# Optimization experiments

Hardware: AMD Instinct MI355X
Metric: run time of the kernel (lower is better)

## Reference

```python
import jax, jax.numpy as jnp
import numpy as np
from jax import lax
from jax.scipy.special import gammaln

B, S, I, H, T, C, LOC, K, P = 64, 256, 512, 80, 600, 512, 8, 21, 11
A_PRIOR, B_PRIOR = 0.1, 0.9
DN = ('NCH', 'OIH', 'NCH')  # 1D conv dimension numbers


def _beta_binom_prior():
    # beta-binomial pmf over P points (n = P-1), flipped to match the torch buffer
    n = float(P - 1)
    k = jnp.arange(P, dtype=jnp.float32)
    lpmf = (gammaln(n + 1.0) - gammaln(k + 1.0) - gammaln(n - k + 1.0)
            + gammaln(k + A_PRIOR) + gammaln(n - k + B_PRIOR) - gammaln(n + A_PRIOR + B_PRIOR)
            - (gammaln(A_PRIOR) + gammaln(B_PRIOR) - gammaln(A_PRIOR + B_PRIOR)))
    return jnp.exp(lpmf)[::-1]


def setup_inputs() -> dict:
    key = jax.random.key(0)
    ks = jax.random.split(key, 10)
    sc = jnp.float32(0.05)
    return {
        'encodings': jax.random.normal(ks[0], (B, S, I), jnp.float32),
        'mask': jnp.ones((B, S), jnp.float32),
        'gt': jax.random.normal(ks[1], (B, T, H), jnp.float32),
        'gru_wi': jax.random.normal(ks[2], (3 * C, I + H), jnp.float32) * sc,
        'gru_wh': jax.random.normal(ks[3], (3 * C, C), jnp.float32) * sc,
        'gru_bi': jnp.zeros((3 * C,), jnp.float32),
        'gru_bh': jnp.zeros((3 * C,), jnp.float32),
        'loc_conv_w': jax.random.normal(ks[4], (LOC, 1, K), jnp.float32) * sc,
        'loc_proj_w': jax.random.normal(ks[5], (C // 2, LOC), jnp.float32) * sc,
        'kernel_w1': jax.random.normal(ks[6], (C, C), jnp.float32) * sc,
        'kernel_b1': jnp.zeros((C,), jnp.float32),
        'kernel_w2': jax.random.normal(ks[7], (LOC * K, C), jnp.float32) * sc,
        'dyn_w': jax.random.normal(ks[8], (C // 2, LOC), jnp.float32) * sc,
        'dyn_b': jnp.zeros((C // 2,), jnp.float32),
        'agg_w': jax.random.normal(ks[9], (C // 2,), jnp.float32) * sc,
        'prior': _beta_binom_prior(),
    }


def reference(encodings, mask, gt, gru_wi, gru_wh, gru_bi, gru_bh,
              loc_conv_w, loc_proj_w, kernel_w1, kernel_b1, kernel_w2,
              dyn_w, dyn_b, agg_w, prior):
    b, s, _ = encodings.shape
    loc, _, k = loc_conv_w.shape
    p = prior.shape[0]
    h0 = jnp.zeros((b, gru_wh.shape[1]), encodings.dtype)
    a0 = jnp.zeros((b, s), encodings.dtype).at[:, 0].set(1.0)

    def step(carry, frame):
        state, alpha = carry
        # attention context from previous alignment
        prev = jnp.einsum('bsi,bs->bi', encodings, alpha)
        x = jnp.concatenate([frame, prev], axis=-1)
        # torch GRUCell gate math
        gx = x @ gru_wi.T + gru_bi
        gh = state @ gru_wh.T + gru_bh
        xr, xz, xn = jnp.split(gx, 3, axis=-1)
        hr, hz, hn = jnp.split(gh, 3, axis=-1)
        r = jax.nn.sigmoid(xr + hr)
        z = jax.nn.sigmoid(xz + hz)
        n = jnp.tanh(xn + r * hn)
        query = (1.0 - z) * n + z * state
        # dynamic kernels predicted from query: [B*loc, 1, K]
        dkern = (jnp.tanh(query @ kernel_w1.T + kernel_b1) @ kernel_w2.T).reshape(b * loc, 1, k)
        pa = alpha[:, None, :]  # [B,1,S]
        # static location conv: [B,loc,S]
        loc_feat = lax.conv_general_dilated(pa, loc_conv_w, (1,), [(k // 2, k // 2)], dimension_numbers=DN)
        # dynamic conv: grouped conv, one filter set per batch element
        dyn_feat = lax.conv_general_dilated(alpha[None], dkern, (1,), [(k // 2, k // 2)],
                                            dimension_numbers=DN, feature_group_count=b).reshape(b, loc, s)
        score = (jnp.einsum('cl,bls->bcs', loc_proj_w, loc_feat)
                 + jnp.einsum('cl,bls->bcs', dyn_w, dyn_feat)
                 + dyn_b[None, :, None])
        # causal prior conv (kernel is pre-flipped beta-binomial pmf)
        pri = lax.conv_general_dilated(pa, prior[None, None, :], (1,), [(p - 1, 0)], dimension_numbers=DN)[:, 0]
        energy = jnp.einsum('c,bcs->bs', agg_w, jnp.tanh(score)) + jnp.log(pri + 1e-5)
        energy = jnp.where(mask > 0, energy, -jnp.inf)
        new_alpha = jax.nn.softmax(energy, axis=-1)
        return (query, new_alpha), new_alpha

    _, alphas = lax.scan(step, (h0, a0), jnp.swapaxes(gt, 0, 1))  # [T,B,S]
    return jnp.swapaxes(alphas, 0, 1)  # [B,T,S]
```

## Files before the change

### kernel.cpp

```cpp
#include <hip/hip_runtime.h>
#include <hip/hip_bf16.h>

#define Bn 64
#define Sn 256
#define In 512
#define Hn 80
#define Tn 600
#define Cn 512
#define LOCn 8
#define Kn 21
#define Pn 11
#define G3 1536

typedef _Float16 h2 __attribute__((ext_vector_type(2)));

enum : unsigned {
  OFF_WHPK     = 0u,
  OFF_W1PK     = OFF_WHPK + 256u * 1536u,
  OFF_W2PK     = OFF_W1PK + 256u * 512u,
  OFF_WIFPK    = OFF_W2PK + 256u * 168u,
  OFF_WIPREVPK = OFF_WIFPK + 40u * 1536u,
  OFF_BI       = OFF_WIPREVPK + 256u * 1536u,
  OFF_BH       = OFF_BI + 1536u,
  OFF_B1       = OFF_BH + 1536u,
  OFF_LW       = OFF_B1 + 512u,
  OFF_PW       = OFF_LW + 176u,
  OFF_DW       = OFF_PW + 2048u,
  OFF_DB       = OFF_DW + 2048u,
  OFF_AGG      = OFF_DB + 256u,
  OFF_PRI      = OFF_AGG + 256u,
  OFF_FLAG     = OFF_PRI + 16u,
  OFF_WIPT     = 1030400u,
  OFF_ENCW     = OFF_WIPT + 512u * 1536u,
  WS_END_ENCW  = OFF_ENCW + 64u * 128u * 1536u,
  OFF_XH       = WS_END_ENCW,
  OFF_TP       = OFF_XH + 64u * 256u,
  OFF_XE       = OFF_TP + 64u * 4096u,
  OFF_FLG      = OFF_XE + 64u * 256u,
  WS_END_ALL   = OFF_FLG + 64u * 32u
};

__device__ __forceinline__ float ld_any(const void* p, long long i, int bf) {
  if (bf) {
    unsigned v = ((const unsigned short*)p)[i];
    return __uint_as_float(v << 16);
  }
  return ((const float*)p)[i];
}
__device__ __forceinline__ unsigned pack_h2(float a, float b) {
  union { h2 h; unsigned u; } x;
  x.h.x = (_Float16)a; x.h.y = (_Float16)b;
  return x.u;
}
__device__ __forceinline__ h2 u_to_h2(unsigned u) {
  union { h2 h; unsigned u; } x; x.u = u; return x.h;
}
__device__ __forceinline__ float dot2f(unsigned w, unsigned a, float acc) {
#if __has_builtin(__builtin_amdgcn_fdot2)
  return __builtin_amdgcn_fdot2(u_to_h2(w), u_to_h2(a), acc, false);
#else
  h2 wv = u_to_h2(w), av = u_to_h2(a);
  return fmaf((float)wv.x, (float)av.x, fmaf((float)wv.y, (float)av.y, acc));
#endif
}

__device__ __forceinline__ void st_dev(unsigned* p, unsigned v) {
  __hip_atomic_store(p, v, __ATOMIC_RELAXED, __HIP_MEMORY_SCOPE_AGENT);
}
__device__ __forceinline__ unsigned ld_dev(const unsigned* p) {
  return __hip_atomic_load(p, __ATOMIC_RELAXED, __HIP_MEMORY_SCOPE_AGENT);
}

__device__ __forceinline__ float fast_exp(float x) {
  return __builtin_amdgcn_exp2f(x * 1.4426950408889634f);
}
__device__ __forceinline__ float fast_sigmoid(float x) {
  return __builtin_amdgcn_rcpf(1.f + fast_exp(-x));
}
__device__ __forceinline__ float fast_tanh(float x) {
  float u = __builtin_amdgcn_exp2f(x * 2.8853900817779268f);
  return 1.f - 2.f * __builtin_amdgcn_rcpf(u + 1.f);
}
__device__ __forceinline__ float fast_log(float x) {
  return __builtin_amdgcn_logf(x) * 0.6931471805599453f;
}

__global__ void k_flag(const void* mask, float* ws) {
  if (threadIdx.x == 0 && blockIdx.x == 0) {
    unsigned w = *(const unsigned*)mask;
    ((int*)(ws + OFF_FLAG))[0] = (w == 0x3F803F80u) ? 1 : 0;
  }
}

__global__ void k_zero(unsigned* U) {
  int x = blockIdx.x * blockDim.x + threadIdx.x;
  if (x < 64 * 32) U[OFF_FLG + x] = 0u;
}

__global__ void k_prep(const void* wi, const void* wh, const void* gbi, const void* gbh,
                       const void* lcw, const void* lpw, const void* w1, const void* kb1,
                       const void* w2, const void* dw, const void* ddb, const void* aggw,
                       const void* pri, float* wsf, unsigned* U) {
  const int bf = ((const int*)(wsf + OFF_FLAG))[0];
  const int tid = blockIdx.x * blockDim.x + threadIdx.x;
  const int nT = gridDim.x * blockDim.x;
  for (int x = tid; x < 256 * 1536; x += nT) {
    int g = x % 3, y = x / 3, c = y % 512, kp = y / 512;
    long long r = (long long)(g * 512 + c) * Cn + 2 * kp;
    U[OFF_WHPK + x] = pack_h2(ld_any(wh, r, bf), ld_any(wh, r + 1, bf));
  }
  for (int x = tid; x < 256 * 512; x += nT) {
    int c = x % 512, kp = x / 512;
    long long r = (long long)c * Cn + 2 * kp;
    U[OFF_W1PK + x] = pack_h2(ld_any(w1, r, bf), ld_any(w1, r + 1, bf));
  }
  for (int x = tid; x < 256 * 168; x += nT) {
    int j = x % 168, kp = x / 168;
    long long r = (long long)j * Cn + 2 * kp;
    U[OFF_W2PK + x] = pack_h2(ld_any(w2, r, bf), ld_any(w2, r + 1, bf));
  }
  for (int x = tid; x < 40 * 1536; x += nT) {
    int g = x % 3, y = x / 3, c = y % 512, jp = y / 512;
    long long r = (long long)(g * 512 + c) * (In + Hn) + 2 * jp;
    U[OFF_WIFPK + x] = pack_h2(ld_any(wi, r, bf), ld_any(wi, r + 1, bf));
  }
  for (int x = tid; x < 256 * 1536; x += nT) {
    int g = x % 3, y = x / 3, c = y % 512, kp = y / 512;
    long long r = (long long)(g * 512 + c) * (In + Hn) + Hn + 2 * kp;
    U[OFF_WIPREVPK + x] = pack_h2(ld_any(wi, r, bf), ld_any(wi, r + 1, bf));
  }
  for (int x = tid; x < 512 * 1536; x += nT) {
    int i = x / 1536, m = x % 1536;
    wsf[OFF_WIPT + x] = ld_any(wi, (long long)m * (In + Hn) + Hn + i, bf);
  }
  for (int x = tid; x < G3; x += nT) wsf[OFF_BI + x] = ld_any(gbi, x, bf);
  for (int x = tid; x < G3; x += nT) wsf[OFF_BH + x] = ld_any(gbh, x, bf);
  for (int x = tid; x < Cn; x += nT) wsf[OFF_B1 + x] = ld_any(kb1, x, bf);
  for (int x = tid; x < LOCn * Kn; x += nT) wsf[OFF_LW + x] = ld_any(lcw, x, bf);
  for (int x = tid; x < 256 * LOCn; x += nT) wsf[OFF_PW + x] = ld_any(lpw, x, bf);
  for (int x = tid; x < 256 * LOCn; x += nT) wsf[OFF_DW + x] = ld_any(dw, x, bf);
  for (int x = tid; x < 256; x += nT) wsf[OFF_DB + x] = ld_any(ddb, x, bf);
  for (int x = tid; x < 256; x += nT) wsf[OFF_AGG + x] = ld_any(aggw, x, bf);
  for (int x = tid; x < Pn; x += nT) wsf[OFF_PRI + x] = ld_any(pri, x, bf);
}

__global__ __launch_bounds__(1024) void k_encw(const void* __restrict__ enc_,
                                               const float* __restrict__ wsf,
                                               unsigned* __restrict__ U) {
  const int b = blockIdx.x >> 2, chunk = blockIdx.x & 3;
  const int bf = ((const int*)(wsf + OFF_FLAG))[0];
  const int tid = threadIdx.x;
  const int r = tid >> 8, m0 = tid & 255;
  const int s0 = chunk * 64 + r * 16;
  const float* WiPT = wsf + OFF_WIPT;
  for (int g6 = 0; g6 < 6; ++g6) {
    int m = m0 + (g6 << 8);
    float acc[16];
    #pragma unroll
    for (int j = 0; j < 16; ++j) acc[j] = 0.f;
    #pragma unroll 4
    for (int i = 0; i < In; ++i) {
      float w = WiPT[(size_t)i * G3 + m];
      #pragma unroll
      for (int j = 0; j < 16; ++j)
        acc[j] = fmaf(w, ld_any(enc_, ((long long)b * Sn + (s0 + j)) * In + i, bf), acc[j]);
    }
    int cc = m & 511, gg = m >> 9;
    unsigned* dst = U + OFF_ENCW + (size_t)b * 128 * G3;
    #pragma unroll
    for (int jj = 0; jj < 8; ++jj)
      dst[(size_t)(((s0 >> 1) + jj) * 512 + cc) * 3 + gg] = pack_h2(acc[2 * jj], acc[2 * jj + 1]);
  }
}

__global__ __launch_bounds__(1024, 4) void k_split(
    const void* __restrict__ mask_, const void* __restrict__ gt_,
    const float* __restrict__ wsf, unsigned* __restrict__ UW,
    void* __restrict__ out_) {
  const int b = blockIdx.x >> 2;
  const int j = blockIdx.x & 3;
  const int tid = threadIdx.x;
  const int bf = ((const int*)(wsf + OFF_FLAG))[0];

  const float* BI = wsf + OFF_BI;
  const float* BH = wsf + OFF_BH;
  const float* B1 = wsf + OFF_B1;
  const float* lw = wsf + OFF_LW;
  const float* Pw = wsf + OFF_PW;
  const float* Dw = wsf + OFF_DW;
  const float* dbv = wsf + OFF_DB;
  const float* agg = wsf + OFF_AGG;
  const float* prw = wsf + OFF_PRI;
  const unsigned* U = UW;
  const unsigned* encwB = U + OFF_ENCW + (size_t)b * 128 * G3;
  unsigned* XH = UW + OFF_XH + b * 256;
  unsigned* TP = UW + OFF_TP + b * 4096;
  unsigned* XE = UW + OFF_XE + b * 256;
  unsigned* FLG = UW + OFF_FLG + b * 32;

  __shared__ __align__(16) float sA[280];
  __shared__ __align__(16) unsigned sAH[128];
  __shared__ __align__(16) unsigned sXfH[40];
  __shared__ __align__(16) unsigned sHH[256];
  __shared__ __align__(16) unsigned sHsl[64];
  __shared__ __align__(16) unsigned sT1H[256];
  __shared__ __align__(16) float sHfC[128];
  __shared__ __align__(16) float sP[6 * 8 * 128];
  __shared__ __align__(16) float sG6[768];
  __shared__ __align__(16) float sFLo[512];
  __shared__ __align__(16) float sFDo[512];
  __shared__ __align__(16) float sPriL[64];
  __shared__ __align__(16) float sDk[176];
  __shared__ __align__(16) float sMask[256];
  __shared__ float sRed2[8];

  for (int x = tid; x < 280; x += 1024) sA[x] = 0.f;
  for (int x = tid; x < 128; x += 1024) { sAH[x] = 0u; sHfC[x & 127] = 0.f; }
  for (int x = tid; x < 256; x += 1024) { sHH[x] = 0u;
    sMask[x] = ld_any(mask_, (long long)b * Sn + x, bf); }
  if (tid == 0) { sA[10] = 1.f; sAH[0] = pack_h2(1.f, 0.f); }
  if (tid < 40) sXfH[tid] = pack_h2(ld_any(gt_, (long long)b * Tn * Hn + 2 * tid, bf),
                                    ld_any(gt_, (long long)b * Tn * Hn + 2 * tid + 1, bf));
  __syncthreads();

  for (int t = 0; t < Tn; ++t) {
    const unsigned ep = (unsigned)(t + 1);
    {
      const int ks = tid >> 7, cl = tid & 127;
      const int c = (j << 7) + cl;
      float xr = 0.f, xz = 0.f, xn = 0.f, hr = 0.f, hz = 0.f, hn = 0.f;
      const unsigned* pf = U + OFF_WIFPK + 3 * c;
      #pragma unroll
      for (int jp = ks * 5; jp < ks * 5 + 5; ++jp) {
        unsigned a = sXfH[jp];
        xr = dot2f(pf[jp * G3], a, xr);
        xz = dot2f(pf[jp * G3 + 1], a, xz);
        xn = dot2f(pf[jp * G3 + 2], a, xn);
      }
      const unsigned* pe = encwB + 3 * c;
      #pragma unroll 4
      for (int kp = ks * 16; kp < ks * 16 + 16; ++kp) {
        unsigned a = sAH[kp];
        if (a) {
          xr = dot2f(pe[kp * G3], a, xr);
          xz = dot2f(pe[kp * G3 + 1], a, xz);
          xn = dot2f(pe[kp * G3 + 2], a, xn);
        }
      }
      const unsigned* ph = U + OFF_WHPK + 3 * c;
      #pragma unroll 4
      for (int kp = ks * 32; kp < ks * 32 + 32; ++kp) {
        unsigned a = sHH[kp];
        hr = dot2f(ph[kp * G3], a, hr);
        hz = dot2f(ph[kp * G3 + 1], a, hz);
        hn = dot2f(ph[kp * G3 + 2], a, hn);
      }
      sP[(0 * 8 + ks) * 128 + cl] = xr;
      sP[(1 * 8 + ks) * 128 + cl] = xz;
      sP[(2 * 8 + ks) * 128 + cl] = xn;
      sP[(3 * 8 + ks) * 128 + cl] = hr;
      sP[(4 * 8 + ks) * 128 + cl] = hz;
      sP[(5 * 8 + ks) * 128 + cl] = hn;
    }
    __syncthreads();
    if (tid < 768) {
      int g = tid >> 7, cl = tid & 127;
      float s = 0.f;
      #pragma unroll
      for (int ks = 0; ks < 8; ++ks) s += sP[(g * 8 + ks) * 128 + cl];
      sG6[tid] = s;
    }
    __syncthreads();
    if (tid < 128) {
      int cl = tid, c = (j << 7) + cl;
      float xr = sG6[cl] + BI[c];
      float xz = sG6[128 + cl] + BI[512 + c];
      float xn = sG6[256 + cl] + BI[1024 + c];
      float hr = sG6[384 + cl] + BH[c];
      float hz = sG6[512 + cl] + BH[512 + c];
      float hn = sG6[640 + cl] + BH[1024 + c];
      float r = fast_sigmoid(xr + hr);
      float z = fast_sigmoid(xz + hz);
      float n = fast_tanh(xn + r * hn);
      float hN = (1.f - z) * n + z * sHfC[cl];
      sHfC[cl] = hN;
      float nb = __shfl_xor(hN, 1, 64);
      if (!(tid & 1)) sHsl[tid >> 1] = pack_h2(hN, nb);
    } else if (tid >= 192 && tid < 256) {
      int sl = tid - 192;
      float acc = 0.f;
      #pragma unroll
      for (int k = 0; k < Pn; ++k) acc = fmaf(prw[k], sA[(j << 6) + sl + k], acc);
      sPriL[sl] = acc;
    } else if (tid >= 512) {
      int idx = tid - 512;
      int l = __builtin_amdgcn_readfirstlane(idx >> 6), sl = idx & 63;
      float acc = 0.f;
      #pragma unroll
      for (int k = 0; k < Kn; ++k) acc = fmaf(lw[l * Kn + k], sA[(j << 6) + sl + k], acc);
      sFLo[l * 64 + sl] = acc;
    }
    __syncthreads();
    {
      const int c = tid & 511, kh = tid >> 9;
      const unsigned* m1 = U + OFF_W1PK + (unsigned)(j * 64 + kh * 32) * 512 + c;
      float acc = 0.f;
      #pragma unroll 4
      for (int kp = 0; kp < 32; ++kp)
        acc = dot2f(m1[kp * 512], sHsl[kh * 32 + kp], acc);
      st_dev(&TP[(j * 2 + kh) * 512 + c], __float_as_uint(acc));
    }
    if (tid < 64) st_dev(&XH[(j << 6) + tid], sHsl[tid]);
    __syncthreads();
    if (tid == 0) st_dev(&FLG[j], ep);
    if (tid < 4) {
      while (ld_dev(&FLG[tid]) < ep) __builtin_amdgcn_s_sleep(1);
    }
    __syncthreads();
    if (tid < 256) sHH[tid] = ld_dev(&XH[tid]);
    if (tid < 512) {
      float a = B1[tid];
      #pragma unroll
      for (int p = 0; p < 8; ++p) a += __uint_as_float(ld_dev(&TP[p * 512 + tid]));
      float tv = fast_tanh(a);
      float nb = __shfl_xor(tv, 1, 64);
      if (!(tid & 1)) sT1H[tid >> 1] = pack_h2(tv, nb);
    }
    __syncthreads();
    if (tid < 672) {
      int kq = tid / 168, j2 = tid - kq * 168;
      const unsigned* m2 = U + OFF_W2PK + kq * 64 * 168 + j2;
      float acc = 0.f;
      #pragma unroll 4
      for (int kp = 0; kp < 64; ++kp)
        acc = dot2f(m2[kp * 168], sT1H[kq * 64 + kp], acc);
      sP[tid] = acc;
    }
    __syncthreads();
    if (tid < 168) sDk[tid] = sP[tid] + sP[tid + 168] + sP[tid + 336] + sP[tid + 504];
    __syncthreads();
    if (tid < 512) {
      int l = __builtin_amdgcn_readfirstlane(tid >> 6), sl = tid & 63;
      float acc = 0.f;
      #pragma unroll
      for (int k = 0; k < Kn; ++k) acc = fmaf(sDk[l * Kn + k], sA[(j << 6) + sl + k], acc);
      sFDo[l * 64 + sl] = acc;
    }
    __syncthreads();
    {
      const int sl = tid & 63;
      const int slice = __builtin_amdgcn_readfirstlane(tid >> 6);
      float fl[LOCn], fd[LOCn];
      #pragma unroll
      for (int l = 0; l < LOCn; ++l) { fl[l] = sFLo[l * 64 + sl]; fd[l] = sFDo[l * 64 + sl]; }
      float e = 0.f;
      const int c0 = slice << 4;
      for (int c = c0; c < c0 + 16; ++c) {
        float sc = dbv[c];
        #pragma unroll
        for (int l = 0; l < LOCn; ++l) {
          sc = fmaf(Pw[c * LOCn + l], fl[l], sc);
          sc = fmaf(Dw[c * LOCn + l], fd[l], sc);
        }
        e = fmaf(agg[c], fast_tanh(sc), e);
      }
      sP[slice * 64 + sl] = e;
    }
    __syncthreads();
    if (tid < 64) {
      float E = 0.f;
      #pragma unroll
      for (int q = 0; q < 16; ++q) E += sP[q * 64 + tid];
      E += fast_log(sPriL[tid] + 1e-5f);
      if (!(sMask[(j << 6) + tid] > 0.f)) E = -__builtin_inff();
      st_dev(&XE[(j << 6) + tid], __float_as_uint(E));
    }
    __builtin_amdgcn_s_waitcnt(0);
    if (tid == 0) st_dev(&FLG[16 + j], ep);
    if (tid < 4) {
      while (ld_dev(&FLG[16 + tid]) < ep) __builtin_amdgcn_s_sleep(1);
    }
    __syncthreads();
    float eV = -__builtin_inff(), exv = 0.f;
    if (tid < 256) {
      eV = __uint_as_float(ld_dev(&XE[tid]));
      float m = eV;
      #pragma unroll
      for (int off = 32; off > 0; off >>= 1) m = fmaxf(m, __shfl_xor(m, off, 64));
      if ((tid & 63) == 0) sRed2[tid >> 6] = m;
    }
    __syncthreads();
    if (tid < 256) {
      float M = fmaxf(fmaxf(sRed2[0], sRed2[1]), fmaxf(sRed2[2], sRed2[3]));
      exv = fast_exp(eV - M);
      float ssum = exv;
      #pragma unroll
      for (int off = 32; off > 0; off >>= 1) ssum += __shfl_xor(ssum, off, 64);
      if ((tid & 63) == 0) sRed2[4 + (tid >> 6)] = ssum;
    } else if (tid >= 512 && tid < 552 && t + 1 < Tn) {
      int i = tid - 512;
      sXfH[i] = pack_h2(ld_any(gt_, ((long long)b * Tn + t + 1) * Hn + 2 * i, bf),
                        ld_any(gt_, ((long long)b * Tn + t + 1) * Hn + 2 * i + 1, bf));
    }
    __syncthreads();
    if (tid < 256) {
      float Z = sRed2[4] + sRed2[5] + sRed2[6] + sRed2[7];
      float a = exv * __builtin_amdgcn_rcpf(Z);
      sA[10 + tid] = a;
      float nb = __shfl_xor(a, 1, 64);
      if (!(tid & 1)) sAH[tid >> 1] = pack_h2(a, nb);
    }
    __syncthreads();
    if (tid >= 256 && tid < 320) {
      int s = (j << 6) + (tid - 256);
      float a = sA[10 + s];
      size_t oi = ((size_t)b * Tn + t) * Sn + s;
      if (bf) ((__hip_bfloat16*)out_)[oi] = __float2bfloat16(a);
      else ((float*)out_)[oi] = a;
    }
    __syncthreads();
  }
}

__global__ __launch_bounds__(1024) void k_single(
    const void* __restrict__ enc_, const void* __restrict__ mask_,
    const void* __restrict__ gt_, const float* __restrict__ wsf,
    const unsigned* __restrict__ U, void* __restrict__ out_, int use_encw) {
  const int b = blockIdx.x;
  const int tid = threadIdx.x;
  const int bf = ((const int*)(wsf + OFF_FLAG))[0];
  const float* BI = wsf + OFF_BI;
  const float* BH = wsf + OFF_BH;
  const float* B1 = wsf + OFF_B1;
  const float* lw = wsf + OFF_LW;
  const float* Pw = wsf + OFF_PW;
  const float* Dw = wsf + OFF_DW;
  const float* dbv = wsf + OFF_DB;
  const float* agg = wsf + OFF_AGG;
  const float* prw = wsf + OFF_PRI;

  __shared__ __align__(16) float sA[280];
  __shared__ __align__(16) unsigned sAH[128];
  __shared__ __align__(16) unsigned sXfH[40];
  __shared__ __align__(16) unsigned sPrevH[256];
  __shared__ __align__(16) float sHf[512];
  __shared__ __align__(16) unsigned sHH[256];
  __shared__ __align__(16) unsigned sT1H[256];
  __shared__ __align__(16) float sXr[512], sXz[512], sXn[512];
  __shared__ __align__(16) float sHr[512], sHz[512], sHnM[512], sHnP[512];
  __shared__ __align__(16) float sDk[176];
  __shared__ __align__(16) float sFL[LOCn][Sn];
  __shared__ __align__(16) float sFD[LOCn][Sn];
  __shared__ __align__(16) float sPri[Sn];
  __shared__ __align__(16) float sMask[Sn];
  __shared__ __align__(16) float sR[1024];
  __shared__ float sRed2[8];

  for (int x = tid; x < 280; x += 1024) sA[x] = 0.f;
  for (int x = tid; x < 128; x += 1024) sAH[x] = 0u;
  for (int x = tid; x < Cn; x += 1024) sHf[x] = 0.f;
  for (int x = tid; x < 256; x += 1024) sHH[x] = 0u;
  for (int x = tid; x < Sn; x += 1024) sMask[x] = ld_any(mask_, (long long)b * Sn + x, bf);
  if (tid == 0) { sA[Kn / 2] = 1.f; sAH[0] = pack_h2(1.f, 0.f); }
  if (tid < Hn) ((_Float16*)sXfH)[tid] = (_Float16)ld_any(gt_, (long long)b * Tn * Hn + tid, bf);
  __syncthreads();

  const int Pp = use_encw ? 132 : 0;
  const int n3 = 256 - Pp;
  const int n1 = use_encw ? 128 : 256;
  const unsigned* encwB = U + OFF_ENCW + (size_t)b * 128 * G3;

  for (int t = 0; t < Tn; ++t) {
    if (!use_encw) {
      int i = tid & (In - 1);
      int s0 = (tid >> 9) << 7;
      float acc = 0.f;
      if (bf) {
        const unsigned short* enc = (const unsigned short*)enc_ + (size_t)b * Sn * In + i;
        #pragma unroll 4
        for (int s = s0; s < s0 + 128; ++s)
          acc = fmaf(__uint_as_float(((unsigned)enc[(size_t)s * In]) << 16), sA[10 + s], acc);
      } else {
        const float* enc = (const float*)enc_ + (size_t)b * Sn * In + i;
        #pragma unroll 4
        for (int s = s0; s < s0 + 128; ++s)
          acc = fmaf(enc[(size_t)s * In], sA[10 + s], acc);
      }
      sR[tid] = acc;
      __syncthreads();
      if (tid < In) ((_Float16*)sPrevH)[tid] = (_Float16)(sR[tid] + sR[tid + In]);
      __syncthreads();
    }
    if (tid < Cn) {
      const int c = tid;
      float xr = BI[c], xz = BI[c + 512], xn = BI[c + 1024];
      {
        const unsigned* pf = U + OFF_WIFPK + 3 * c;
        #pragma unroll 4
        for (int jp = 0; jp < 40; ++jp) {
          unsigned a = sXfH[jp];
          xr = dot2f(pf[jp * G3], a, xr);
          xz = dot2f(pf[jp * G3 + 1], a, xz);
          xn = dot2f(pf[jp * G3 + 2], a, xn);
        }
      }
      {
        const unsigned* pm = use_encw ? (encwB + 3 * c) : (U + OFF_WIPREVPK + 3 * c);
        const unsigned* aSrc = use_encw ? sAH : sPrevH;
        #pragma unroll 4
        for (int kp = 0; kp < n1; ++kp) {
          unsigned a = aSrc[kp];
          xr = dot2f(pm[kp * G3], a, xr);
          xz = dot2f(pm[kp * G3 + 1], a, xz);
          xn = dot2f(pm[kp * G3 + 2], a, xn);
        }
      }
      {
        float hp = 0.f;
        const unsigned* ph = U + OFF_WHPK + 3 * c + 2;
        #pragma unroll 4
        for (int kp = n3; kp < 256; ++kp)
          hp = dot2f(ph[kp * G3], sHH[kp], hp);
        sHnP[c] = hp;
      }
      sXr[c] = xr; sXz[c] = xz; sXn[c] = xn;
    } else {
      const int c = tid - Cn;
      float hr = BH[c], hz = BH[c + 512], hn = BH[c + 1024];
      const unsigned* ph = U + OFF_WHPK + 3 * c;
      #pragma unroll 4
      for (int kp = 0; kp < n3; ++kp) {
        unsigned a = sHH[kp];
        hr = dot2f(ph[kp * G3], a, hr);
        hz = dot2f(ph[kp * G3 + 1], a, hz);
        hn = dot2f(ph[kp * G3 + 2], a, hn);
      }
      #pragma unroll 4
      for (int kp = n3; kp < 256; ++kp) {
        unsigned a = sHH[kp];
        hr = dot2f(ph[kp * G3], a, hr);
        hz = dot2f(ph[kp * G3 + 1], a, hz);
      }
      sHr[c] = hr; sHz[c] = hz; sHnM[c] = hn;
    }
    __syncthreads();
    if (tid < Cn) {
      int c = tid;
      float r = fast_sigmoid(sXr[c] + sHr[c]);
      float z = fast_sigmoid(sXz[c] + sHz[c]);
      float n = fast_tanh(sXn[c] + r * (sHnM[c] + sHnP[c]));
      float hN = (1.f - z) * n + z * sHf[c];
      sHf[c] = hN;
      ((_Float16*)sHH)[c] = (_Float16)hN;
    } else {
      int j = tid - Cn;
      #pragma unroll
      for (int rr = 0; rr < 4; ++rr) {
        int idx = j + (rr << 9);
        int l = idx >> 8, s = idx & (Sn - 1);
        float acc = 0.f;
        #pragma unroll
        for (int k = 0; k < Kn; ++k) acc = fmaf(lw[l * Kn + k], sA[s + k], acc);
        sFL[l][s] = acc;
      }
      if (j < Sn) {
        float acc = 0.f;
        #pragma unroll
        for (int k = 0; k < Pn; ++k) acc = fmaf(prw[k], sA[j + k], acc);
        sPri[j] = acc;
      }
    }
    __syncthreads();
    {
      int c = tid & (Cn - 1), half = tid >> 9;
      const unsigned* m1 = U + OFF_W1PK + half * 128 * 512 + c;
      float acc = 0.f;
      #pragma unroll 4
      for (int kp = 0; kp < 128; ++kp)
        acc = dot2f(m1[kp * 512], sHH[half * 128 + kp], acc);
      sR[tid] = acc;
    }
    __syncthreads();
    if (tid < Cn) ((_Float16*)sT1H)[tid] = (_Float16)fast_tanh(B1[tid] + sR[tid] + sR[tid + Cn]);
    __syncthreads();
    if (tid < 672) {
      int kq = tid / 168, j = tid - kq * 168;
      const unsigned* m2 = U + OFF_W2PK + kq * 64 * 168 + j;
      float acc = 0.f;
      #pragma unroll 4
      for (int kp = 0; kp < 64; ++kp)
        acc = dot2f(m2[kp * 168], sT1H[kq * 64 + kp], acc);
      sR[tid] = acc;
    }
    __syncthreads();
    if (tid < LOCn * Kn) sDk[tid] = sR[tid] + sR[tid + 168] + sR[tid + 336] + sR[tid + 504];
    __syncthreads();
    #pragma unroll
    for (int rr = 0; rr < 2; ++rr) {
      int idx = tid + (rr << 10);
      int l = idx >> 8, s = idx & (Sn - 1);
      float acc = 0.f;
      #pragma unroll
      for (int k = 0; k < Kn; ++k) acc = fmaf(sDk[l * Kn + k], sA[s + k], acc);
      sFD[l][s] = acc;
    }
    __syncthreads();
    {
      const int q = __builtin_amdgcn_readfirstlane(tid >> 8);
      const int s = tid & (Sn - 1);
      float fl0[LOCn], fd0[LOCn];
      #pragma unroll
      for (int l = 0; l < LOCn; ++l) { fl0[l] = sFL[l][s]; fd0[l] = sFD[l][s]; }
      float e = 0.f;
      const int c0 = q << 6;
      for (int c = c0; c < c0 + 64; ++c) {
        float sc = dbv[c];
        #pragma unroll
        for (int l = 0; l < LOCn; ++l) {
          sc = fmaf(Pw[c * LOCn + l], fl0[l], sc);
          sc = fmaf(Dw[c * LOCn + l], fd0[l], sc);
        }
        e = fmaf(agg[c], fast_tanh(sc), e);
      }
      sR[tid] = e;
    }
    __syncthreads();
    float eVal = -__builtin_inff();
    if (tid < Sn) {
      eVal = sR[tid] + sR[tid + 256] + sR[tid + 512] + sR[tid + 768];
      eVal += fast_log(sPri[tid] + 1e-5f);
      if (!(sMask[tid] > 0.f)) eVal = -__builtin_inff();
      float m = eVal;
      #pragma unroll
      for (int off = 32; off > 0; off >>= 1) m = fmaxf(m, __shfl_xor(m, off, 64));
      if ((tid & 63) == 0) sRed2[tid >> 6] = m;
    }
    __syncthreads();
    float exv = 0.f;
    if (tid < Sn) {
      float M = fmaxf(fmaxf(sRed2[0], sRed2[1]), fmaxf(sRed2[2], sRed2[3]));
      exv = fast_exp(eVal - M);
      float ssum = exv;
      #pragma unroll
      for (int off = 32; off > 0; off >>= 1) ssum += __shfl_xor(ssum, off, 64);
      if ((tid & 63) == 0) sRed2[4 + (tid >> 6)] = ssum;
    }
    __syncthreads();
    if (tid < Sn) {
      float Z = sRed2[4] + sRed2[5] + sRed2[6] + sRed2[7];
      float a = exv * __builtin_amdgcn_rcpf(Z);
      sA[10 + tid] = a;
      ((_Float16*)sAH)[tid] = (_Float16)a;
      size_t oi = ((size_t)b * Tn + t) * Sn + tid;
      if (bf) ((__hip_bfloat16*)out_)[oi] = __float2bfloat16(a);
      else ((float*)out_)[oi] = a;
    } else if (tid >= 512 && tid < 512 + Hn && t + 1 < Tn) {
      int j = tid - 512;
      ((_Float16*)sXfH)[j] = (_Float16)ld_any(gt_, ((long long)b * Tn + t + 1) * Hn + j, bf);
    }
    __syncthreads();
  }
}

extern "C" void kernel_launch(void* const* d_in, const int* in_sizes, int n_in,
                              void* d_out, int out_size, void* d_ws, size_t ws_size,
                              hipStream_t stream) {
  float* wsf = (float*)d_ws;
  unsigned* U = (unsigned*)d_ws;
  const int use_encw = (ws_size >= (size_t)WS_END_ENCW * 4u) ? 1 : 0;
  const int use_split = (ws_size >= (size_t)WS_END_ALL * 4u) ? 1 : 0;
  k_flag<<<1, 64, 0, stream>>>(d_in[1], wsf);
  k_prep<<<1024, 256, 0, stream>>>(d_in[3], d_in[4], d_in[5], d_in[6],
                                   d_in[7], d_in[8], d_in[9], d_in[10],
                                   d_in[11], d_in[12], d_in[13], d_in[14],
                                   d_in[15], wsf, U);
  if (use_split) {
    k_encw<<<256, 1024, 0, stream>>>(d_in[0], wsf, U);
    k_zero<<<8, 256, 0, stream>>>(U);
    k_split<<<256, 1024, 0, stream>>>(d_in[1], d_in[2], wsf, U, d_out);
  } else {
    if (use_encw) k_encw<<<256, 1024, 0, stream>>>(d_in[0], wsf, U);
    k_single<<<Bn, 1024, 0, stream>>>(d_in[0], d_in[1], d_in[2], wsf, U, d_out, use_encw);
  }
}
```

Baseline: 18.71 ms.

## Compact nonzero alpha indices and batch weight loads in split GRU kernel

Builds a compacted list of nonzero packed alpha pairs with a wave ballot, so the encoder-weighted GRU input projection loops only over nonzero entries instead of testing every one. It also preloads weight chunks into register arrays before the dot products in the GRU, W1 and W2 matvecs, giving more loads in flight. The block index mapping is changed so the four blocks of one batch element are spread across the grid, and the global partial-sum loads are batched. The cost is a dynamic, divergent loop trip count, extra register pressure from the weight buffers, and one extra synchronisation step to pack alpha.

```diff
diff --git a/kernel.cpp b/kernel.cpp
--- a/kernel.cpp
+++ b/kernel.cpp
@@ -177,8 +177,8 @@
     const void* __restrict__ mask_, const void* __restrict__ gt_,
     const float* __restrict__ wsf, unsigned* __restrict__ UW,
     void* __restrict__ out_) {
-  const int b = blockIdx.x >> 2;
-  const int j = blockIdx.x & 3;
+  const int b = blockIdx.x & 63;
+  const int j = blockIdx.x >> 6;
   const int tid = threadIdx.x;
   const int bf = ((const int*)(wsf + OFF_FLAG))[0];
 
@@ -212,13 +212,15 @@
   __shared__ __align__(16) float sPriL[64];
   __shared__ __align__(16) float sDk[176];
   __shared__ __align__(16) float sMask[256];
+  __shared__ int sIdx[128];
+  __shared__ int sNz;
   __shared__ float sRed2[8];
 
   for (int x = tid; x < 280; x += 1024) sA[x] = 0.f;
   for (int x = tid; x < 128; x += 1024) { sAH[x] = 0u; sHfC[x & 127] = 0.f; }
   for (int x = tid; x < 256; x += 1024) { sHH[x] = 0u;
     sMask[x] = ld_any(mask_, (long long)b * Sn + x, bf); }
-  if (tid == 0) { sA[10] = 1.f; sAH[0] = pack_h2(1.f, 0.f); }
+  if (tid == 0) { sA[10] = 1.f; sAH[0] = pack_h2(1.f, 0.f); sIdx[0] = 0; sNz = 1; }
   if (tid < 40) sXfH[tid] = pack_h2(ld_any(gt_, (long long)b * Tn * Hn + 2 * tid, bf),
                                     ld_any(gt_, (long long)b * Tn * Hn + 2 * tid + 1, bf));
   __syncthreads();
@@ -229,31 +231,55 @@
       const int ks = tid >> 7, cl = tid & 127;
       const int c = (j << 7) + cl;
       float xr = 0.f, xz = 0.f, xn = 0.f, hr = 0.f, hz = 0.f, hn = 0.f;
-      const unsigned* pf = U + OFF_WIFPK + 3 * c;
-      #pragma unroll
-      for (int jp = ks * 5; jp < ks * 5 + 5; ++jp) {
-        unsigned a = sXfH[jp];
-        xr = dot2f(pf[jp * G3], a, xr);
-        xz = dot2f(pf[jp * G3 + 1], a, xz);
-        xn = dot2f(pf[jp * G3 + 2], a, xn);
-      }
-      const unsigned* pe = encwB + 3 * c;
-      #pragma unroll 4
-      for (int kp = ks * 16; kp < ks * 16 + 16; ++kp) {
-        unsigned a = sAH[kp];
-        if (a) {
-          xr = dot2f(pe[kp * G3], a, xr);
-          xz = dot2f(pe[kp * G3 + 1], a, xz);
-          xn = dot2f(pe[kp * G3 + 2], a, xn);
+      {
+        const unsigned* pf = U + OFF_WIFPK + 3 * c;
+        unsigned w[15];
+        #pragma unroll
+        for (int q = 0; q < 5; ++q) {
+          w[3 * q]     = pf[(ks * 5 + q) * G3];
+          w[3 * q + 1] = pf[(ks * 5 + q) * G3 + 1];
+          w[3 * q + 2] = pf[(ks * 5 + q) * G3 + 2];
         }
-      }
-      const unsigned* ph = U + OFF_WHPK + 3 * c;
-      #pragma unroll 4
-      for (int kp = ks * 32; kp < ks * 32 + 32; ++kp) {
-        unsigned a = sHH[kp];
-        hr = dot2f(ph[kp * G3], a, hr);
-        hz = dot2f(ph[kp * G3 + 1], a, hz);
-        hn = dot2f(ph[kp * G3 + 2], a, hn);
+        #pragma unroll
+        for (int q = 0; q < 5; ++q) {
+          unsigned a = sXfH[ks * 5 + q];
+          xr = dot2f(w[3 * q], a, xr);
+          xz = dot2f(w[3 * q + 1], a, xz);
+          xn = dot2f(w[3 * q + 2], a, xn);
+        }
+      }
+      {
+        const unsigned* pe = encwB + 3 * c;
+        const int m = sNz;
+        for (int ii = ks; ii < m; ii += 8) {
+          int kp = sIdx[ii];
+          unsigned a = sAH[kp];
+          unsigned w0 = pe[kp * G3], w1 = pe[kp * G3 + 1], w2 = pe[kp * G3 + 2];
+          xr = dot2f(w0, a, xr);
+          xz = dot2f(w1, a, xz);
+          xn = dot2f(w2, a, xn);
+        }
+      }
+      {
+        const unsigned* ph = U + OFF_WHPK + 3 * c;
+        #pragma unroll
+        for (int ch = 0; ch < 4; ++ch) {
+          const int k0 = ks * 32 + ch * 8;
+          unsigned w[24];
+          #pragma unroll
+          for (int q = 0; q < 8; ++q) {
+            w[3 * q]     = ph[(k0 + q) * G3];
+            w[3 * q + 1] = ph[(k0 + q) * G3 + 1];
+            w[3 * q + 2] = ph[(k0 + q) * G3 + 2];
+          }
+          #pragma unroll
+          for (int q = 0; q < 8; ++q) {
+            unsigned a = sHH[k0 + q];
+            hr = dot2f(w[3 * q], a, hr);
+            hz = dot2f(w[3 * q + 1], a, hz);
+            hn = dot2f(w[3 * q + 2], a, hn);
+          }
+        }
       }
       sP[(0 * 8 + ks) * 128 + cl] = xr;
       sP[(1 * 8 + ks) * 128 + cl] = xz;
@@ -305,9 +331,15 @@
       const int c = tid & 511, kh = tid >> 9;
       const unsigned* m1 = U + OFF_W1PK + (unsigned)(j * 64 + kh * 32) * 512 + c;
       float acc = 0.f;
-      #pragma unroll 4
-      for (int kp = 0; kp < 32; ++kp)
-        acc = dot2f(m1[kp * 512], sHsl[kh * 32 + kp], acc);
+      #pragma unroll
+      for (int ch = 0; ch < 2; ++ch) {
+        unsigned w[16];
+        #pragma unroll
+        for (int q = 0; q < 16; ++q) w[q] = m1[(ch * 16 + q) * 512];
+        #pragma unroll
+        for (int q = 0; q < 16; ++q)
+          acc = dot2f(w[q], sHsl[kh * 32 + ch * 16 + q], acc);
+      }
       st_dev(&TP[(j * 2 + kh) * 512 + c], __float_as_uint(acc));
     }
     if (tid < 64) st_dev(&XH[(j << 6) + tid], sHsl[tid]);
@@ -319,9 +351,12 @@
     __syncthreads();
     if (tid < 256) sHH[tid] = ld_dev(&XH[tid]);
     if (tid < 512) {
+      unsigned v[8];
+      #pragma unroll
+      for (int p = 0; p < 8; ++p) v[p] = ld_dev(&TP[p * 512 + tid]);
       float a = B1[tid];
       #pragma unroll
-      for (int p = 0; p < 8; ++p) a += __uint_as_float(ld_dev(&TP[p * 512 + tid]));
+      for (int p = 0; p < 8; ++p) a += __uint_as_float(v[p]);
       float tv = fast_tanh(a);
       float nb = __shfl_xor(tv, 1, 64);
       if (!(tid & 1)) sT1H[tid >> 1] = pack_h2(tv, nb);
@@ -331,9 +366,15 @@
       int kq = tid / 168, j2 = tid - kq * 168;
       const unsigned* m2 = U + OFF_W2PK + kq * 64 * 168 + j2;
       float acc = 0.f;
-      #pragma unroll 4
-      for (int kp = 0; kp < 64; ++kp)
-        acc = dot2f(m2[kp * 168], sT1H[kq * 64 + kp], acc);
+      #pragma unroll
+      for (int ch = 0; ch < 4; ++ch) {
+        unsigned w[16];
+        #pragma unroll
+        for (int q = 0; q < 16; ++q) w[q] = m2[(ch * 16 + q) * 168];
+        #pragma unroll
+        for (int q = 0; q < 16; ++q)
+          acc = dot2f(w[q], sT1H[kq * 64 + ch * 16 + q], acc);
+      }
       sP[tid] = acc;
     }
     __syncthreads();
@@ -405,13 +446,23 @@
     __syncthreads();
     if (tid < 256) {
       float Z = sRed2[4] + sRed2[5] + sRed2[6] + sRed2[7];
-      float a = exv * __builtin_amdgcn_rcpf(Z);
-      sA[10 + tid] = a;
-      float nb = __shfl_xor(a, 1, 64);
-      if (!(tid & 1)) sAH[tid >> 1] = pack_h2(a, nb);
-    }
-    __syncthreads();
-    if (tid >= 256 && tid < 320) {
+      sA[10 + tid] = exv * __builtin_amdgcn_rcpf(Z);
+    }
+    __syncthreads();
+    if (tid < 64) {
+      float a0 = sA[10 + 4 * tid], a1 = sA[10 + 4 * tid + 1];
+      float a2 = sA[10 + 4 * tid + 2], a3 = sA[10 + 4 * tid + 3];
+      unsigned p0 = pack_h2(a0, a1), p1 = pack_h2(a2, a3);
+      sAH[2 * tid] = p0;
+      sAH[2 * tid + 1] = p1;
+      unsigned long long m0 = __ballot(p0 != 0u);
+      unsigned long long m1 = __ballot(p1 != 0u);
+      unsigned long long lt = (1ull << tid) - 1ull;
+      int pos = __popcll(m0 & lt) + __popcll(m1 & lt);
+      if (p0) sIdx[pos++] = 2 * tid;
+      if (p1) sIdx[pos] = 2 * tid + 1;
+      if (tid == 0) sNz = __popcll(m0) + __popcll(m1);
+    } else if (tid >= 256 && tid < 320) {
       int s = (j << 6) + (tid - 256);
       float a = sA[10 + s];
       size_t oi = ((size_t)b * Tn + t) * Sn + s;
```

Measured after the change: 44.21 ms. 136% more time.
